# Performance work log

Measured on AMD Instinct MI355X. Metric: run time of the kernel, lower is better.

## Reference

```python
import jax, jax.numpy as jnp
import numpy as np

A0, A1, A2 = 1.0, 1.0, 0.5  # Taylor coefficients of exp around 0 (p=2)

B, H, N, D = 2, 16, 4096, 32


def setup_inputs() -> dict:
    key = jax.random.key(0)
    kq, kk, kv = jax.random.split(key, 3)
    q = jax.random.normal(kq, (B, H, N, D), dtype=jnp.float32)
    k = jax.random.normal(kk, (B, H, N, D), dtype=jnp.float32)
    v = jax.random.normal(kv, (B, H, N, D), dtype=jnp.float32)
    return {"q": q, "k": k, "v": v}


def reference(q, k, v):
    # fastmax_function with p=2, mask=False, normalize=False, dropout=0 -> temperature=1
    b, h, n, d = q.shape
    # quadratic feature maps: flatten of outer products, [b,h,n,d*d]
    q2 = (q[..., :, None] * q[..., None, :]).reshape(b, h, n, d * d)
    k2 = (k[..., :, None] * k[..., None, :]).reshape(b, h, n, d * d)
    # numerator: a0*sum(v) + a1*q(k^T v) + a2*q2(k2^T v)
    second_term = A1 * jnp.einsum('bhnd,bhne->bhde', k, v)           # [b,h,d,d]
    third_term = A2 * jnp.einsum('bhnf,bhne->bhfe', k2, v)           # [b,h,d^2,d]
    ans = (jnp.einsum('bhnd,bhde->bhne', q, second_term)
           + jnp.einsum('bhnf,bhfe->bhne', q2, third_term)
           + A0 * jnp.sum(v, axis=-2, keepdims=True))                 # [b,h,n,d]
    # denominator: a0*n + a1*q.sum(k) + a2*q2.sum(k2)
    div = (A0 * n
           + A1 * jnp.einsum('bhnd,bhd->bhn', q, jnp.sum(k, axis=-2))
           + A2 * jnp.einsum('bhnf,bhf->bhn', q2, jnp.sum(k2, axis=-2)))  # [b,h,n]
    return ans / div[..., None]
```

## Files before the change

kernel.cpp:

```cpp
#include <hip/hip_runtime.h>

#define NTOK 4096
#define NBH  32
#define NF   1088
#define NE   33
#define GTF_BH 52224

typedef _Float16 half_t;
typedef _Float16 half8 __attribute__((ext_vector_type(8)));
typedef _Float16 half4v __attribute__((ext_vector_type(4)));
typedef float f32x4 __attribute__((ext_vector_type(4)));
typedef unsigned int u32;

#define MFMA16(A,B,C) __builtin_amdgcn_mfma_f32_16x16x32_f16((A),(B),(C),0,0,0)

#define ASYNC_CP16(dst_lds, src_glb) \
    __builtin_amdgcn_global_load_lds( \
        (const __attribute__((address_space(1))) u32*)(const void*)(src_glb), \
        (__attribute__((address_space(3))) u32*)(void*)(dst_lds), 16, 0, 0)

static __device__ __forceinline__ half8 splat8(half_t x) {
    return (half8){x, x, x, x, x, x, x, x};
}

__global__ __launch_bounds__(256)
void t_kernel(const float* __restrict__ kin, const float* __restrict__ vin,
              half_t* __restrict__ kTg, half_t* __restrict__ vTg)
{
    const int nb = blockIdx.x;
    const int bh = blockIdx.y;
    const int t  = threadIdx.x;
    __shared__ __align__(16) half_t tile[32 * 272];
    const size_t inbase = ((size_t)bh * NTOK + nb * 256) * 32;

    for (int pass = 0; pass < 2; ++pass) {
        const float* src = pass ? vin : kin;
        half_t* dstg     = pass ? vTg : kTg;
        if (pass) __syncthreads();
        const float4* s4 = (const float4*)(src + inbase);
        #pragma unroll
        for (int r = 0; r < 8; ++r) {
            int f4 = t + 256 * r;
            int n = f4 >> 3, d4 = f4 & 7;
            float4 vv = s4[f4];
            int nn = n ^ ((d4 & 7) << 3);
            int d0 = d4 * 4;
            tile[(d0 + 0) * 272 + nn] = (half_t)vv.x;
            tile[(d0 + 1) * 272 + nn] = (half_t)vv.y;
            tile[(d0 + 2) * 272 + nn] = (half_t)vv.z;
            tile[(d0 + 3) * 272 + nn] = (half_t)vv.w;
        }
        __syncthreads();
        #pragma unroll
        for (int cc = 0; cc < 4; ++cc) {
            int lin = t + 256 * cc;
            int d = lin >> 5, ch = lin & 31;
            int sw = (d >> 2) & 7;
            half8 val = *(const half8*)&tile[d * 272 + ((ch ^ sw) << 3)];
            *(half8*)&dstg[((size_t)bh * 32 + d) * NTOK + nb * 256 + ch * 8] = val;
        }
    }
}

template<int NMT>
__device__ __forceinline__ void a_body(
    const half_t* __restrict__ kTg, const half_t* __restrict__ vTg,
    half_t* __restrict__ P, int Kc, int bh, int kc, int pw,
    int t, int w, int l16, int quad, half_t* kT0, half_t* vT0)
{
    const half8 h05 = splat8((half_t)0.5f);
    f32x4 acc[NMT][3];
    #pragma unroll
    for (int m = 0; m < NMT; ++m)
        #pragma unroll
        for (int e = 0; e < 3; ++e)
            acc[m][e] = (f32x4){0.f, 0.f, 0.f, 0.f};

    const size_t gbase = (size_t)bh * 32 * NTOK;
    const int nPer = NTOK / Kc;
    const int nStages = nPer >> 7;

    const int c0 = t,        r0 = c0 >> 4, p0s = (c0 & 15) ^ (r0 & 15);
    const int c1 = 256 + t,  r1 = c1 >> 4, p1s = (c1 & 15) ^ (r1 & 15);

    auto issue = [&](int buf, int nbase) {
        const half_t* gk0 = kTg + gbase + (size_t)r0 * NTOK + nbase + p0s * 8;
        const half_t* gk1 = kTg + gbase + (size_t)r1 * NTOK + nbase + p1s * 8;
        const half_t* gv0 = vTg + gbase + (size_t)r0 * NTOK + nbase + p0s * 8;
        const half_t* gv1 = vTg + gbase + (size_t)r1 * NTOK + nbase + p1s * 8;
        half_t* kb = kT0 + buf * 4096;
        half_t* vb = vT0 + buf * 4096;
        ASYNC_CP16(kb + (size_t)w * 512,        gk0);
        ASYNC_CP16(kb + 2048 + (size_t)w * 512, gk1);
        ASYNC_CP16(vb + (size_t)w * 512,        gv0);
        ASYNC_CP16(vb + 2048 + (size_t)w * 512, gv1);
    };

    issue(0, kc * nPer);

    for (int st = 0; st < nStages; ++st) {
        const int cur = st & 1;
        __syncthreads();
        if (st + 1 < nStages) issue(cur ^ 1, kc * nPer + (st + 1) * 128);
        const half_t* kb = kT0 + cur * 4096;
        const half_t* vb = vT0 + cur * 4096;
        #pragma unroll
        for (int kk = 0; kk < 4; ++kk) {
            const int c = kk * 4 + quad;
            const int shL = ((c ^ l16) << 3);
            half8 kj0 = *(const half8*)&kb[l16 * 128 + shL];
            half8 kj1 = *(const half8*)&kb[(l16 + 16) * 128 + shL];
            half8 bf0 = *(const half8*)&vb[l16 * 128 + shL];
            half8 bf1 = *(const half8*)&vb[(l16 + 16) * 128 + shL];
            half_t onec = (l16 == 0) ? (half_t)1 : (half_t)0;
            half8 bf2 = {onec, onec, onec, onec, onec, onec, onec, onec};
            #pragma unroll
            for (int mt = 0; mt < NMT; ++mt) {
                const int pm = pw + mt * 16;
                half8 af;
                if (pm < 32) {
                    af = pm ? kj1 : kj0;
                } else if (pm == 1056) {
                    af = bf2;
                } else if (pm > 1056) {
                    continue;
                } else {
                    const int i = (pm - 32) >> 5;
                    const int j0 = (pm - 32) & 31;
                    half8 ki = *(const half8*)&kb[i * 128 + ((c ^ (i & 15)) << 3)];
                    ki = ki * h05;
                    af = ki * (j0 ? kj1 : kj0);
                }
                acc[mt][0] = MFMA16(af, bf0, acc[mt][0]);
                acc[mt][1] = MFMA16(af, bf1, acc[mt][1]);
                acc[mt][2] = MFMA16(af, bf2, acc[mt][2]);
            }
        }
    }

    half_t* Pb = P + ((size_t)kc * NBH + bh) * NE * NF;
    #pragma unroll
    for (int mt = 0; mt < NMT; ++mt) {
        int p0 = pw + mt * 16 + quad * 4;
        half4v h0 = {(half_t)acc[mt][0][0], (half_t)acc[mt][0][1],
                     (half_t)acc[mt][0][2], (half_t)acc[mt][0][3]};
        half4v h1 = {(half_t)acc[mt][1][0], (half_t)acc[mt][1][1],
                     (half_t)acc[mt][1][2], (half_t)acc[mt][1][3]};
        *(half4v*)&Pb[(size_t)l16 * NF + p0] = h0;
        *(half4v*)&Pb[(size_t)(l16 + 16) * NF + p0] = h1;
        if (l16 == 0) {
            half4v h2 = {(half_t)acc[mt][2][0], (half_t)acc[mt][2][1],
                         (half_t)acc[mt][2][2], (half_t)acc[mt][2][3]};
            *(half4v*)&Pb[(size_t)32 * NF + p0] = h2;
        }
    }
}

__global__ __launch_bounds__(256, 2)
void a_kernel(const half_t* __restrict__ kTg, const half_t* __restrict__ vTg,
              half_t* __restrict__ P, int Kc)
{
    const int x  = blockIdx.x;
    const int bh = x & (NBH - 1);
    const int kc = x >> 5;
    const int half = blockIdx.y;
    const int t = threadIdx.x;
    const int w = t >> 6, lane = t & 63, l16 = lane & 15, quad = lane >> 4;

    __shared__ __align__(16) half_t kT[2 * 4096];
    __shared__ __align__(16) half_t vT[2 * 4096];

    if (half == 0) {
        a_body<9>(kTg, vTg, P, Kc, bh, kc, w * 144, t, w, l16, quad, kT, vT);
    } else {
        a_body<8>(kTg, vTg, P, Kc, bh, kc, 576 + w * 128, t, w, l16, quad, kT, vT);
    }
}

__global__ __launch_bounds__(256)
void ar_kernel(const half_t* __restrict__ P, half_t* __restrict__ GtF, int Kc)
{
    const int NP8 = NBH * NE * NF / 8;
    const int idx = blockIdx.x * 256 + threadIdx.x;
    if (idx >= NP8) return;
    float s[8] = {0.f, 0.f, 0.f, 0.f, 0.f, 0.f, 0.f, 0.f};
    for (int c = 0; c < Kc; ++c) {
        half8 h = *(const half8*)&P[(size_t)c * (NBH * NE * NF) + (size_t)idx * 8];
        #pragma unroll
        for (int j = 0; j < 8; ++j) s[j] += (float)h[j];
    }
    half8 o;
    #pragma unroll
    for (int j = 0; j < 8; ++j) o[j] = (half_t)s[j];
    int row = idx / 136;
    int p8 = idx - row * 136;
    int e = row % 33, bhh = row / 33;
    int kt = p8 >> 2, quad = p8 & 3;
    int rr = e >> 4, l16 = e & 15;
    size_t dst8 = (size_t)bhh * (GTF_BH / 8)
                + (size_t)(kt * 3 + rr) * 64 + quad * 16 + l16;
    *(half8*)&GtF[dst8 * 8] = o;
}

__global__ __launch_bounds__(256)
void b_kernel(const float* __restrict__ qin, const half_t* __restrict__ GtF,
              float* __restrict__ out)
{
    const int bh = blockIdx.x, mbq = blockIdx.y;
    const int t = threadIdx.x, w = t >> 6, lane = t & 63;
    const int l16 = lane & 15, quad = lane >> 4;
    __shared__ __align__(16) half_t qs[256 * 40];
    __shared__ __align__(16) half_t qsP[32 * 272];
    __shared__ float denl[256];
    const size_t nbase = (size_t)bh * NTOK + mbq * 256;

    const float4* q4 = (const float4*)(qin + nbase * 32);
    #pragma unroll
    for (int r = 0; r < 8; ++r) {
        int f4 = t + 256 * r, n = f4 >> 3, d4 = f4 & 7;
        float4 vv = q4[f4];
        half4v h = {(half_t)vv.x, (half_t)vv.y, (half_t)vv.z, (half_t)vv.w};
        *(half4v*)&qs[n * 40 + d4 * 4] = h;
        int pb = (n >> 6) * 64 + (n & 15) * 4 + ((n >> 4) & 3);
        qsP[(4 * d4 + 0) * 272 + pb] = h[0];
        qsP[(4 * d4 + 1) * 272 + pb] = h[1];
        qsP[(4 * d4 + 2) * 272 + pb] = h[2];
        qsP[(4 * d4 + 3) * 272 + pb] = h[3];
    }
    __syncthreads();

    const int rbase = w * 64;
    half8 vq[4];
    #pragma unroll
    for (int mt = 0; mt < 4; ++mt)
        vq[mt] = *(const half8*)&qs[(rbase + mt * 16 + l16) * 40 + quad * 8];

    f32x4 acc[3][4];
    #pragma unroll
    for (int a = 0; a < 3; ++a)
        #pragma unroll
        for (int b = 0; b < 4; ++b)
            acc[a][b] = (f32x4){0.f, 0.f, 0.f, 0.f};

    const half_t* Gb = GtF + (size_t)bh * GTF_BH + (size_t)lane * 8;
    const int sOff = w * 64 + l16 * 4;

#define LDF(kt, B) do { \
    _Pragma("unroll") \
    for (int rr = 0; rr < 3; ++rr) \
        (B)[rr] = *(const half8*)&Gb[(size_t)(((kt) * 3 + rr) * 64) * 8]; \
} while (0)

    half8 B0[3], B1[3], B2[3], B3[3];
    LDF(0, B0); LDF(1, B1); LDF(2, B2);

    {
        LDF(3, B3);
        #pragma unroll
        for (int mt = 0; mt < 4; ++mt) {
            acc[0][mt] = MFMA16(vq[mt], B0[0], acc[0][mt]);
            acc[1][mt] = MFMA16(vq[mt], B0[1], acc[1][mt]);
            acc[2][mt] = MFMA16(vq[mt], B0[2], acc[2][mt]);
        }
        #pragma unroll
        for (int rr = 0; rr < 3; ++rr) { B0[rr] = B1[rr]; B1[rr] = B2[rr]; B2[rr] = B3[rr]; }
    }
    #pragma unroll 1
    for (int kt = 1; kt <= 32; ++kt) {
        const int ktp = (kt + 3 <= 33) ? kt + 3 : 33;
        LDF(ktp, B3);
        half4v sv = *(const half4v*)&qsP[(kt - 1) * 272 + sOff];
        half8 af[4];
        #pragma unroll
        for (int mt = 0; mt < 4; ++mt)
            af[mt] = vq[mt] * splat8(sv[mt]);
        #pragma unroll
        for (int mt = 0; mt < 4; ++mt) {
            acc[0][mt] = MFMA16(af[mt], B0[0], acc[0][mt]);
            acc[1][mt] = MFMA16(af[mt], B0[1], acc[1][mt]);
            acc[2][mt] = MFMA16(af[mt], B0[2], acc[2][mt]);
        }
        #pragma unroll
        for (int rr = 0; rr < 3; ++rr) { B0[rr] = B1[rr]; B1[rr] = B2[rr]; B2[rr] = B3[rr]; }
    }
    {
        half8 cf = {};
        if (quad == 0) cf[0] = (half_t)1;
        #pragma unroll
        for (int mt = 0; mt < 4; ++mt) {
            acc[0][mt] = MFMA16(cf, B0[0], acc[0][mt]);
            acc[1][mt] = MFMA16(cf, B0[1], acc[1][mt]);
            acc[2][mt] = MFMA16(cf, B0[2], acc[2][mt]);
        }
    }
#undef LDF

    if (l16 == 0) {
        #pragma unroll
        for (int mt = 0; mt < 4; ++mt)
            #pragma unroll
            for (int r = 0; r < 4; ++r)
                denl[rbase + mt * 16 + quad * 4 + r] = acc[2][mt][r];
    }
    __syncthreads();
    #pragma unroll
    for (int mt = 0; mt < 4; ++mt) {
        float inv[4];
        #pragma unroll
        for (int r = 0; r < 4; ++r)
            inv[r] = __builtin_amdgcn_rcpf(denl[rbase + mt * 16 + quad * 4 + r]);
        #pragma unroll
        for (int r = 0; r < 4; ++r) {
            size_t ro = (nbase + rbase + mt * 16 + quad * 4 + r) * 32;
            out[ro + l16] = acc[0][mt][r] * inv[r];
            out[ro + l16 + 16] = acc[1][mt][r] * inv[r];
        }
    }
}

extern "C" void kernel_launch(void* const* d_in, const int* in_sizes, int n_in,
                              void* d_out, int out_size, void* d_ws, size_t ws_size,
                              hipStream_t stream)
{
    const float* q = (const float*)d_in[0];
    const float* k = (const float*)d_in[1];
    const float* v = (const float*)d_in[2];
    float* out = (float*)d_out;

    const size_t planeBytes = (size_t)NBH * NE * NF * 2;
    const size_t ktBytes = (size_t)NBH * 32 * NTOK * 2;
    const size_t gtBytes = (size_t)NBH * GTF_BH * 2;
    int Kc = 8;
    while (Kc > 1 && ((size_t)Kc * planeBytes + 2 * ktBytes + gtBytes) > ws_size)
        Kc >>= 1;

    half_t* P = (half_t*)d_ws;
    half_t* kTg = (half_t*)((char*)d_ws + (size_t)Kc * planeBytes);
    half_t* vTg = kTg + (size_t)NBH * 32 * NTOK;
    half_t* GtF = vTg + (size_t)NBH * 32 * NTOK;

    t_kernel<<<dim3(16, NBH), 256, 0, stream>>>(k, v, kTg, vTg);
    a_kernel<<<dim3(Kc * NBH, 2), 256, 0, stream>>>(kTg, vTg, P, Kc);
    ar_kernel<<<561, 256, 0, stream>>>(P, GtF, Kc);
    b_kernel<<<dim3(NBH, 16), 256, 0, stream>>>(q, GtF, out);
}
```

Before: 138.4 us.

## Exploit symmetry of quadratic features to halve feature dimension

Replaces the full d*d outer-product feature space (1024 + linear + const = 1088 columns) with its symmetric half (i<j pairs via cyclic rotation, plus diagonal terms), reducing features to 576. The a_kernel now builds rotated k_i*k_j products per 16-row tile and the b_kernel builds matching q_i*q_{i+s} features via register shuffles from a duplicated q layout. This roughly halves MFMA work and partial-plane traffic in both the reduction and apply stages. The split count Kc is also raised to 16 to keep parallelism now that the a_kernel has a single grid half.

```diff
diff --git a/kernel.cpp b/kernel.cpp
--- a/kernel.cpp
+++ b/kernel.cpp
@@ -2,9 +2,10 @@
 
 #define NTOK 4096
 #define NBH  32
-#define NF   1088
+#define NF   576
 #define NE   33
-#define GTF_BH 52224
+#define NKT  18
+#define GTF_BH (NKT * 3 * 64 * 8)
 
 typedef _Float16 half_t;
 typedef _Float16 half8 __attribute__((ext_vector_type(8)));
@@ -62,19 +63,43 @@
     }
 }
 
-template<int NMT>
-__device__ __forceinline__ void a_body(
-    const half_t* __restrict__ kTg, const half_t* __restrict__ vTg,
-    half_t* __restrict__ P, int Kc, int bh, int kc, int pw,
-    int t, int w, int l16, int quad, half_t* kT0, half_t* vT0)
-{
+__global__ __launch_bounds__(256, 2)
+void a_kernel(const half_t* __restrict__ kTg, const half_t* __restrict__ vTg,
+              half_t* __restrict__ P, int Kc)
+{
+    const int x  = blockIdx.x;
+    const int bh = x & (NBH - 1);
+    const int kc = x >> 5;
+    const int t = threadIdx.x;
+    const int w = t >> 6, lane = t & 63, l16 = lane & 15, quad = lane >> 4;
+    const int pw = w * 144;
+
+    __shared__ __align__(16) half_t kT0[2 * 4096];
+    __shared__ __align__(16) half_t vT0[2 * 4096];
+
     const half8 h05 = splat8((half_t)0.5f);
-    f32x4 acc[NMT][3];
-    #pragma unroll
-    for (int m = 0; m < NMT; ++m)
+    f32x4 acc[9][3];
+    #pragma unroll
+    for (int m = 0; m < 9; ++m)
         #pragma unroll
         for (int e = 0; e < 3; ++e)
             acc[m][e] = (f32x4){0.f, 0.f, 0.f, 0.f};
+
+    int rotoff[9], rotsalt[9];
+    #pragma unroll
+    for (int mt = 0; mt < 9; ++mt) {
+        const int pm = pw + mt * 16;
+        int ro = 0, rs = 0;
+        if (pm >= 32 && pm < 512) {
+            const int s  = 1 + ((pm - 32) >> 5);
+            const int i0 = (pm - 32) & 31;
+            const int r  = (i0 + l16 + s) & 31;
+            ro = r * 128;
+            rs = r & 15;
+        }
+        rotoff[mt] = ro;
+        rotsalt[mt] = rs;
+    }
 
     const size_t gbase = (size_t)bh * 32 * NTOK;
     const int nPer = NTOK / Kc;
@@ -113,23 +138,24 @@
             half8 bf0 = *(const half8*)&vb[l16 * 128 + shL];
             half8 bf1 = *(const half8*)&vb[(l16 + 16) * 128 + shL];
             half_t onec = (l16 == 0) ? (half_t)1 : (half_t)0;
-            half8 bf2 = {onec, onec, onec, onec, onec, onec, onec, onec};
+            half8 bf2 = splat8(onec);
             #pragma unroll
-            for (int mt = 0; mt < NMT; ++mt) {
+            for (int mt = 0; mt < 9; ++mt) {
                 const int pm = pw + mt * 16;
                 half8 af;
                 if (pm < 32) {
                     af = pm ? kj1 : kj0;
-                } else if (pm == 1056) {
+                } else if (pm < 512) {
+                    half8 rot = *(const half8*)&kb[rotoff[mt] + ((c ^ rotsalt[mt]) << 3)];
+                    af = (((pm - 32) & 16) ? kj1 : kj0) * rot;
+                } else if (pm == 512) {
+                    af = kj0 * kj1;
+                } else if (pm == 528) {
+                    af = (kj0 * h05) * kj0;
+                } else if (pm == 544) {
+                    af = (kj1 * h05) * kj1;
+                } else {
                     af = bf2;
-                } else if (pm > 1056) {
-                    continue;
-                } else {
-                    const int i = (pm - 32) >> 5;
-                    const int j0 = (pm - 32) & 31;
-                    half8 ki = *(const half8*)&kb[i * 128 + ((c ^ (i & 15)) << 3)];
-                    ki = ki * h05;
-                    af = ki * (j0 ? kj1 : kj0);
                 }
                 acc[mt][0] = MFMA16(af, bf0, acc[mt][0]);
                 acc[mt][1] = MFMA16(af, bf1, acc[mt][1]);
@@ -140,7 +166,7 @@
 
     half_t* Pb = P + ((size_t)kc * NBH + bh) * NE * NF;
     #pragma unroll
-    for (int mt = 0; mt < NMT; ++mt) {
+    for (int mt = 0; mt < 9; ++mt) {
         int p0 = pw + mt * 16 + quad * 4;
         half4v h0 = {(half_t)acc[mt][0][0], (half_t)acc[mt][0][1],
                      (half_t)acc[mt][0][2], (half_t)acc[mt][0][3]};
@@ -156,27 +182,6 @@
     }
 }
 
-__global__ __launch_bounds__(256, 2)
-void a_kernel(const half_t* __restrict__ kTg, const half_t* __restrict__ vTg,
-              half_t* __restrict__ P, int Kc)
-{
-    const int x  = blockIdx.x;
-    const int bh = x & (NBH - 1);
-    const int kc = x >> 5;
-    const int half = blockIdx.y;
-    const int t = threadIdx.x;
-    const int w = t >> 6, lane = t & 63, l16 = lane & 15, quad = lane >> 4;
-
-    __shared__ __align__(16) half_t kT[2 * 4096];
-    __shared__ __align__(16) half_t vT[2 * 4096];
-
-    if (half == 0) {
-        a_body<9>(kTg, vTg, P, Kc, bh, kc, w * 144, t, w, l16, quad, kT, vT);
-    } else {
-        a_body<8>(kTg, vTg, P, Kc, bh, kc, 576 + w * 128, t, w, l16, quad, kT, vT);
-    }
-}
-
 __global__ __launch_bounds__(256)
 void ar_kernel(const half_t* __restrict__ P, half_t* __restrict__ GtF, int Kc)
 {
@@ -192,8 +197,8 @@
     half8 o;
     #pragma unroll
     for (int j = 0; j < 8; ++j) o[j] = (half_t)s[j];
-    int row = idx / 136;
-    int p8 = idx - row * 136;
+    int row = idx / 72;
+    int p8 = idx - row * 72;
     int e = row % 33, bhh = row / 33;
     int kt = p8 >> 2, quad = p8 & 3;
     int rr = e >> 4, l16 = e & 15;
@@ -209,8 +214,7 @@
     const int bh = blockIdx.x, mbq = blockIdx.y;
     const int t = threadIdx.x, w = t >> 6, lane = t & 63;
     const int l16 = lane & 15, quad = lane >> 4;
-    __shared__ __align__(16) half_t qs[256 * 40];
-    __shared__ __align__(16) half_t qsP[32 * 272];
+    __shared__ __align__(16) half_t qs2[256 * 56];
     __shared__ float denl[256];
     const size_t nbase = (size_t)bh * NTOK + mbq * 256;
 
@@ -220,20 +224,24 @@
         int f4 = t + 256 * r, n = f4 >> 3, d4 = f4 & 7;
         float4 vv = q4[f4];
         half4v h = {(half_t)vv.x, (half_t)vv.y, (half_t)vv.z, (half_t)vv.w};
-        *(half4v*)&qs[n * 40 + d4 * 4] = h;
-        int pb = (n >> 6) * 64 + (n & 15) * 4 + ((n >> 4) & 3);
-        qsP[(4 * d4 + 0) * 272 + pb] = h[0];
-        qsP[(4 * d4 + 1) * 272 + pb] = h[1];
-        qsP[(4 * d4 + 2) * 272 + pb] = h[2];
-        qsP[(4 * d4 + 3) * 272 + pb] = h[3];
+        *(half4v*)&qs2[n * 56 + d4 * 4] = h;
+        if (d4 < 4) *(half4v*)&qs2[n * 56 + 32 + d4 * 4] = h;
     }
     __syncthreads();
 
     const int rbase = w * 64;
-    half8 vq[4];
-    #pragma unroll
-    for (int mt = 0; mt < 4; ++mt)
-        vq[mt] = *(const half8*)&qs[(rbase + mt * 16 + l16) * 40 + quad * 8];
+    int tb[4];
+    #pragma unroll
+    for (int mt = 0; mt < 4; ++mt) tb[mt] = (rbase + mt * 16 + l16) * 56;
+
+    half8 vq[4], hv[4], gv[4];
+    #pragma unroll
+    for (int mt = 0; mt < 4; ++mt) {
+        const int qb = tb[mt] + quad * 8;
+        vq[mt] = *(const half8*)&qs2[qb];
+        hv[mt] = *(const half8*)&qs2[qb + 8];
+        gv[mt] = *(const half8*)&qs2[qb + 16];
+    }
 
     f32x4 acc[3][4];
     #pragma unroll
@@ -243,7 +251,6 @@
             acc[a][b] = (f32x4){0.f, 0.f, 0.f, 0.f};
 
     const half_t* Gb = GtF + (size_t)bh * GTF_BH + (size_t)lane * 8;
-    const int sOff = w * 64 + l16 * 4;
 
 #define LDF(kt, B) do { \
     _Pragma("unroll") \
@@ -251,48 +258,75 @@
         (B)[rr] = *(const half8*)&Gb[(size_t)(((kt) * 3 + rr) * 64) * 8]; \
 } while (0)
 
+#define DO_MFMA(AF) do { \
+    _Pragma("unroll") \
+    for (int mt = 0; mt < 4; ++mt) { \
+        acc[0][mt] = MFMA16((AF)[mt], B0[0], acc[0][mt]); \
+        acc[1][mt] = MFMA16((AF)[mt], B0[1], acc[1][mt]); \
+        acc[2][mt] = MFMA16((AF)[mt], B0[2], acc[2][mt]); \
+    } \
+} while (0)
+
+#define RING() do { \
+    _Pragma("unroll") \
+    for (int rr = 0; rr < 3; ++rr) { B0[rr] = B1[rr]; B1[rr] = B2[rr]; B2[rr] = B3[rr]; } \
+} while (0)
+
     half8 B0[3], B1[3], B2[3], B3[3];
     LDF(0, B0); LDF(1, B1); LDF(2, B2);
 
     {
         LDF(3, B3);
+        DO_MFMA(vq);
+        RING();
+    }
+
+#define QCHUNK(S) do { \
+    if ((S) + 3 <= 17) LDF((S) + 3, B3); \
+    half8 af[4]; \
+    _Pragma("unroll") \
+    for (int mt = 0; mt < 4; ++mt) { \
+        half8 lo = ((S) < 8) ? vq[mt] : hv[mt]; \
+        half8 hi = ((S) < 8) ? hv[mt] : gv[mt]; \
+        half8 rot = __builtin_shufflevector(lo, hi, \
+            ((S) & 7) + 0, ((S) & 7) + 1, ((S) & 7) + 2, ((S) & 7) + 3, \
+            ((S) & 7) + 4, ((S) & 7) + 5, ((S) & 7) + 6, ((S) & 7) + 7); \
+        af[mt] = vq[mt] * rot; \
+    } \
+    DO_MFMA(af); \
+    RING(); \
+} while (0)
+
+    QCHUNK(1);  QCHUNK(2);  QCHUNK(3);  QCHUNK(4);  QCHUNK(5);
+    QCHUNK(6);  QCHUNK(7);  QCHUNK(8);  QCHUNK(9);  QCHUNK(10);
+    QCHUNK(11); QCHUNK(12); QCHUNK(13); QCHUNK(14); QCHUNK(15);
+
+    {
+        half8 af[4];
         #pragma unroll
         for (int mt = 0; mt < 4; ++mt) {
-            acc[0][mt] = MFMA16(vq[mt], B0[0], acc[0][mt]);
-            acc[1][mt] = MFMA16(vq[mt], B0[1], acc[1][mt]);
-            acc[2][mt] = MFMA16(vq[mt], B0[2], acc[2][mt]);
-        }
-        #pragma unroll
-        for (int rr = 0; rr < 3; ++rr) { B0[rr] = B1[rr]; B1[rr] = B2[rr]; B2[rr] = B3[rr]; }
-    }
-    #pragma unroll 1
-    for (int kt = 1; kt <= 32; ++kt) {
-        const int ktp = (kt + 3 <= 33) ? kt + 3 : 33;
-        LDF(ktp, B3);
-        half4v sv = *(const half4v*)&qsP[(kt - 1) * 272 + sOff];
+            const int off = tb[mt] + ((quad >= 2) ? (quad - 2) : quad) * 8;
+            half8 Ld = *(const half8*)&qs2[off];
+            af[mt] = (quad < 2) ? (vq[mt] * gv[mt]) : (Ld * Ld);
+        }
+        DO_MFMA(af);
+        RING();
+    }
+    {
+        const half8 zero = {};
+        half8 c10 = {};
+        c10[0] = (half_t)1;
         half8 af[4];
         #pragma unroll
-        for (int mt = 0; mt < 4; ++mt)
-            af[mt] = vq[mt] * splat8(sv[mt]);
-        #pragma unroll
         for (int mt = 0; mt < 4; ++mt) {
-            acc[0][mt] = MFMA16(af[mt], B0[0], acc[0][mt]);
-            acc[1][mt] = MFMA16(af[mt], B0[1], acc[1][mt]);
-            acc[2][mt] = MFMA16(af[mt], B0[2], acc[2][mt]);
-        }
-        #pragma unroll
-        for (int rr = 0; rr < 3; ++rr) { B0[rr] = B1[rr]; B1[rr] = B2[rr]; B2[rr] = B3[rr]; }
-    }
-    {
-        half8 cf = {};
-        if (quad == 0) cf[0] = (half_t)1;
-        #pragma unroll
-        for (int mt = 0; mt < 4; ++mt) {
-            acc[0][mt] = MFMA16(cf, B0[0], acc[0][mt]);
-            acc[1][mt] = MFMA16(cf, B0[1], acc[1][mt]);
-            acc[2][mt] = MFMA16(cf, B0[2], acc[2][mt]);
-        }
-    }
+            half8 d = gv[mt] * gv[mt];
+            af[mt] = (quad < 2) ? d : ((quad == 2) ? c10 : zero);
+        }
+        DO_MFMA(af);
+    }
+#undef QCHUNK
+#undef RING
+#undef DO_MFMA
 #undef LDF
 
     if (l16 == 0) {
@@ -330,7 +364,7 @@
     const size_t planeBytes = (size_t)NBH * NE * NF * 2;
     const size_t ktBytes = (size_t)NBH * 32 * NTOK * 2;
     const size_t gtBytes = (size_t)NBH * GTF_BH * 2;
-    int Kc = 8;
+    int Kc = 16;
     while (Kc > 1 && ((size_t)Kc * planeBytes + 2 * ktBytes + gtBytes) > ws_size)
         Kc >>= 1;
 
@@ -340,7 +374,8 @@
     half_t* GtF = vTg + (size_t)NBH * 32 * NTOK;
 
     t_kernel<<<dim3(16, NBH), 256, 0, stream>>>(k, v, kTg, vTg);
-    a_kernel<<<dim3(Kc * NBH, 2), 256, 0, stream>>>(kTg, vTg, P, Kc);
-    ar_kernel<<<561, 256, 0, stream>>>(P, GtF, Kc);
+    a_kernel<<<dim3(Kc * NBH), 256, 0, stream>>>(kTg, vTg, P, Kc);
+    const int NP8 = NBH * NE * NF / 8;
+    ar_kernel<<<(NP8 + 255) / 256, 256, 0, stream>>>(P, GtF, Kc);
     b_kernel<<<dim3(NBH, 16), 256, 0, stream>>>(q, GtF, out);
 }
```

New measurement: 126.6 us. 1.09x faster.
